# Optimization experiments

Measured on AMD Instinct MI355X. Metric: run time of the kernel, lower is better.

Reference implementation:

```python
import jax, jax.numpy as jnp
import numpy as np

U10_IDX, V10_IDX = 0, 1
WIND_THRESH = 0.5


def _gru(x, h, Wih, Whh, bih, bhh):
    # standard torch GRUCell math
    gi = x @ Wih.T + bih
    gh = h @ Whh.T + bhh
    ir, iz, inn = jnp.split(gi, 3, axis=-1)
    hr, hz, hnn = jnp.split(gh, 3, axis=-1)
    r = jax.nn.sigmoid(ir + hr)
    z = jax.nn.sigmoid(iz + hz)
    n = jnp.tanh(inn + r * hnn)
    return (1.0 - z) * n + z * h


def setup_inputs() -> dict:
    B, N, H, F, Th, Tf = 256, 184, 128, 8, 24, 24
    key = jax.random.key(0)
    ks = jax.random.split(key, 24)
    s = 0.1
    f32 = jnp.float32
    feature = jax.random.normal(ks[0], (B, Th + Tf, N, F), f32)
    pm25_hist = jax.random.uniform(ks[1], (B, Th, N, 1), dtype=f32)
    adj_mat = (jax.random.uniform(ks[2], (N, N)) < 0.1).astype(f32)
    angles = jax.random.uniform(ks[3], (N, N), f32, 0.0, 2.0 * np.pi)
    C = F + 1  # ChebConv in-channels = in_dim + out_dim
    return dict(
        feature=feature, pm25_hist=pm25_hist, adj_mat=adj_mat, angles=angles,
        W_ih_hist=s * jax.random.normal(ks[4], (3 * H, 2), f32),
        W_hh_hist=s * jax.random.normal(ks[5], (3 * H, H), f32),
        b_ih_hist=s * jax.random.normal(ks[6], (3 * H,), f32),
        b_hh_hist=s * jax.random.normal(ks[7], (3 * H,), f32),
        fc_hist_w=s * jax.random.normal(ks[8], (1, H), f32),
        fc_hist_b=s * jax.random.normal(ks[9], (1,), f32),
        cheb_w0=s * jax.random.normal(ks[10], (C, 1), f32),
        cheb_w1=s * jax.random.normal(ks[11], (C, 1), f32),
        cheb_b=s * jax.random.normal(ks[12], (1,), f32),
        W_ih=s * jax.random.normal(ks[13], (3 * H, C + 1), f32),
        W_hh=s * jax.random.normal(ks[14], (3 * H, H), f32),
        b_ih=s * jax.random.normal(ks[15], (3 * H,), f32),
        b_hh=s * jax.random.normal(ks[16], (3 * H,), f32),
        fc_out_w=s * jax.random.normal(ks[17], (1, H), f32),
        fc_out_b=s * jax.random.normal(ks[18], (1,), f32),
    )


def reference(feature, pm25_hist, adj_mat, angles,
              W_ih_hist, W_hh_hist, b_ih_hist, b_hh_hist,
              fc_hist_w, fc_hist_b,
              cheb_w0, cheb_w1, cheb_b,
              W_ih, W_hh, b_ih, b_hh,
              fc_out_w, fc_out_b):
    B, T, N, F = feature.shape
    H = W_hh.shape[1]
    Th = pm25_hist.shape[1]
    comp1 = jnp.cos(angles)                                # [N,N]
    comp2 = jnp.cos(angles - jnp.float32(np.pi / 2.0))     # [N,N]
    adj_b = adj_mat > 0

    # ---- history GRU over pm25_hist ----
    def hist_step(carry, p):
        hn, xn = carry
        x = jnp.concatenate([xn, p], axis=-1).reshape(B * N, 2)
        hn = _gru(x, hn, W_ih_hist, W_hh_hist, b_ih_hist, b_hh_hist)
        xn = hn.reshape(B, N, H) @ fc_hist_w.T + fc_hist_b
        return (hn, xn), None

    h0 = jnp.zeros((B * N, H), feature.dtype)
    x0 = jnp.zeros((B, N, 1), feature.dtype)
    (hn, xn), _ = jax.lax.scan(hist_step, (h0, x0), jnp.swapaxes(pm25_hist, 0, 1))

    # ---- forecast: dynamic wind-gated graph + ChebConv(K=2) + GRU ----
    def fore_step(carry, f):
        hn, xn = carry
        x = jnp.concatenate([xn, f], axis=-1)              # [B,N,F+1]
        u = f[..., U10_IDX]                                # [B,N]
        v = f[..., V10_IDX]
        wind = u[:, :, None] * comp1[None] + v[:, :, None] * comp2[None]
        # edge i->j iff adj and wind projection >= threshold
        M = jnp.logical_and(wind >= WIND_THRESH, adj_b[None]).astype(x.dtype)
        deg = M.sum(-1)                                    # source degree [B,N]
        has = deg > 0
        dinv = jnp.where(has, 1.0 / jnp.sqrt(jnp.where(has, deg, 1.0)), 0.0)
        # ChebConv scaled Laplacian (lambda_max=2, sym norm):
        # L_hat x [j] = -dinv_j * sum_i dinv_i * M[i,j] * x[i] + (0 if deg_j>0 else -1) * x[j]
        y = jnp.einsum('bij,bic->bjc', M * dinv[:, :, None], x)
        y = -dinv[:, :, None] * y + jnp.where(has, 0.0, -1.0)[:, :, None] * x
        g = jax.nn.sigmoid(x @ cheb_w0 + y @ cheb_w1 + cheb_b)  # [B,N,1]
        x2 = jnp.concatenate([x, g], axis=-1).reshape(B * N, F + 2)
        hn = _gru(x2, hn, W_ih, W_hh, b_ih, b_hh)
        xn = hn.reshape(B, N, H) @ fc_out_w.T + fc_out_b
        return (hn, xn), xn

    fore_feat = jnp.swapaxes(feature[:, Th:], 0, 1)        # [Tf,B,N,F]
    (_, _), preds = jax.lax.scan(fore_step, (hn, xn), fore_feat)
    return jnp.swapaxes(preds, 0, 1)                       # [B,Tf,N,1]
```

## Files before the change

### kernel.cpp

```cpp
#include <hip/hip_runtime.h>
#include <hip/hip_bf16.h>
#include <math.h>

#define BB 256
#define NN 184
#define HH 128
#define FF 8
#define TH 24
#define TF 24
#define KA 160
#define NG 512
#define RPAD 192
#define STRH 136
#define NT 1024
#define NW3 552
#define LOG2E 1.44269504088896f

#define REC_F 8832
#define REC_H 2944
#define OFF_DINV 4416
#define OFF_G 5152
#define OFF_AXF 5888

typedef __attribute__((ext_vector_type(8))) short bf16x8;
typedef __attribute__((ext_vector_type(4))) short bf16x4;
typedef __attribute__((ext_vector_type(4))) float f32x4;
typedef __attribute__((ext_vector_type(2))) unsigned u32x2;

#if __has_builtin(__builtin_amdgcn_mfma_f32_16x16x16bf16_1k)
#define XK16 1
#else
#define XK16 0
#endif

__host__ __device__ __forceinline__ long recOff(int b, int t) {
    const long PB = (long)TH * REC_H + (long)TF * REC_F;
    return (long)b * PB + ((t < TH) ? (long)t * REC_H
                                    : (long)TH * REC_H + (long)(t - TH) * REC_F);
}

__device__ __forceinline__ unsigned short f2bf(float f) {
    unsigned u = __float_as_uint(f);
    u += 0x7fffu + ((u >> 16) & 1u);
    return (unsigned short)(u >> 16);
}
__device__ __forceinline__ unsigned pkbf(float a, float b) {
    __hip_bfloat162 h = __float22bfloat162_rn(make_float2(a, b));
    return *reinterpret_cast<unsigned*>(&h);
}
__device__ __forceinline__ void gload16(const void* src, void* dst) {
    __builtin_amdgcn_global_load_lds(
        (const __attribute__((address_space(1))) unsigned int*)src,
        (__attribute__((address_space(3))) unsigned int*)dst, 16, 0, 0);
}

__global__ void prep_weights(const float* __restrict__ WhhH, const float* __restrict__ WihH,
                             const float* __restrict__ WhhF, const float* __restrict__ WihF,
                             const float* __restrict__ bihH, const float* __restrict__ bhhH,
                             const float* __restrict__ bihF, const float* __restrict__ bhhF,
                             unsigned short* __restrict__ WaH, unsigned short* __restrict__ WaF) {
    int idx = blockIdx.x * 256 + threadIdx.x;
    if (idx >= NG * KA) return;
    int jp = idx / KA, k = idx % KA;
    int j = jp & 127, part = jp >> 7;
    float vh = 0.f, vf = 0.f;
    if (part <= 1) {
        int row = part * 128 + j;
        if (k < 128) { vh = WhhH[row * 128 + k]; vf = WhhF[row * 128 + k]; }
        else {
            int s = k - 128;
            if (s == 0)  vh = WihH[row * 2 + 1];
            if (s < 8)   vf = WihF[row * 10 + (s + 1)];
            if (s == 8)  { vh = WihH[row * 2 + 0]; vf = WihF[row * 10 + 0]; }
            if (s == 9)  vf = WihF[row * 10 + 9];
            if (s == 11) { vh = bihH[row] + bhhH[row]; vf = bihF[row] + bhhF[row]; }
        }
    } else if (part == 2) {
        if (k < 128) { vh = WhhH[(256 + j) * 128 + k]; vf = WhhF[(256 + j) * 128 + k]; }
        else if (k == 139) { vh = bhhH[256 + j]; vf = bhhF[256 + j]; }
    } else {
        if (k >= 128) {
            int s = k - 128;
            if (s == 0)  vh = WihH[(256 + j) * 2 + 1];
            if (s < 8)   vf = WihF[(256 + j) * 10 + (s + 1)];
            if (s == 8)  { vh = WihH[(256 + j) * 2 + 0]; vf = WihF[(256 + j) * 10 + 0]; }
            if (s == 9)  vf = WihF[(256 + j) * 10 + 9];
            if (s == 11) { vh = bihH[256 + j]; vf = bihF[256 + j]; }
        }
    }
    float sc = (part <= 1) ? LOG2E : 2.0f * LOG2E;
    WaH[idx] = f2bf(vh * sc);
    WaF[idx] = f2bf(vf * sc);
}

__global__ void prep_edges(const float* __restrict__ angles, const float* __restrict__ adj,
                           float4* __restrict__ edges, int* __restrict__ cnt) {
    int idx = blockIdx.x * 256 + threadIdx.x;
    if (idx < NN * NN && adj[idx] > 0.f) {
        float a = angles[idx];
        int pos = atomicAdd(cnt, 1);
        float4 r;
        r.x = cosf(a);
        r.y = cosf(a - 1.57079632679489662f);
        r.z = __int_as_float(idx / NN);
        r.w = __int_as_float(idx % NN);
        edges[pos] = r;
    }
}

__global__ __launch_bounds__(256) void prep_graph(
    const float* __restrict__ feature, const float* __restrict__ pm25,
    const float4* __restrict__ edges, const int* __restrict__ ecnt,
    const float* __restrict__ cw0, const float* __restrict__ cw1,
    const float* __restrict__ cbb, char* __restrict__ xrec)
{
    const int bt = blockIdx.x;
    const int b = bt / (TH + TF), tt = bt % (TH + TF);
    const int tid = threadIdx.x;

    char* rec = xrec + recOff(b, tt);
    if (tt < TH) {
        if (tid < NN) {
            unsigned short pb = f2bf(pm25[((long)b * TH + tt) * NN + tid]);
            uint4* dst = (uint4*)rec + tid;
            *dst = make_uint4((unsigned)pb, 0u, 0u, 0u);
        }
        return;
    }

    __shared__ float f8[NN * FF];
    __shared__ unsigned long long mT[NN][3];
    __shared__ int dg[NN];
    __shared__ float di[NN];
    __shared__ float red[NW3][8];

    const float4* fb4 = (const float4*)(feature + ((long)b * (TH + TF) + tt) * (NN * FF));
    for (int i = tid; i < (NN * FF) / 4; i += 256) ((float4*)f8)[i] = fb4[i];
    for (int i = tid; i < NN * 3; i += 256) ((unsigned long long*)mT)[i] = 0ull;
    for (int i = tid; i < NN; i += 256) dg[i] = 0;
    __syncthreads();
    const int nE = *ecnt;
    for (int e = tid; e < nE; e += 256) {
        float4 r = edges[e];
        int ii = __float_as_int(r.z), jj = __float_as_int(r.w);
        if (f8[ii * FF] * r.x + f8[ii * FF + 1] * r.y >= 0.5f) {
            atomicAdd(&dg[ii], 1);
            atomicOr(&mT[jj][ii >> 6], 1ull << (ii & 63));
        }
    }
    __syncthreads();
    if (tid < NN) di[tid] = (dg[tid] > 0) ? rsqrtf((float)dg[tid]) : 0.f;
    __syncthreads();
    unsigned long long* mr = (unsigned long long*)rec;
    for (int i = tid; i < NW3; i += 256) mr[i] = ((const unsigned long long*)mT)[i];
    for (int task = tid; task < NW3; task += 256) {
        int j = task / 3, wd = task - j * 3;
        unsigned long long m = mT[j][wd];
        float acc[8];
        #pragma unroll
        for (int c = 0; c < 8; ++c) acc[c] = 0.f;
        while (m) {
            int bp = __ffsll(m) - 1; m &= m - 1;
            int i = wd * 64 + bp;
            float d = di[i];
            #pragma unroll
            for (int c = 0; c < 8; ++c) acc[c] += d * f8[i * FF + c];
        }
        #pragma unroll
        for (int c = 0; c < 8; ++c) red[task][c] = acc[c];
    }
    __syncthreads();
    if (tid < NN) {
        int j = tid;
        float dj = di[j];
        float hzj = (dj > 0.f) ? 0.f : -1.f;
        float G = cbb[0];
        #pragma unroll
        for (int c = 0; c < 8; ++c) {
            float accc = red[j * 3 + 0][c] + red[j * 3 + 1][c] + red[j * 3 + 2][c];
            float xv = f8[j * FF + c];
            float y = -dj * accc + hzj * xv;
            G += xv * cw0[c + 1] + y * cw1[c + 1];
        }
        ((float*)(rec + OFF_DINV))[j] = dj;
        ((float*)(rec + OFF_G))[j] = G;
        unsigned short* ax = (unsigned short*)(rec + OFF_AXF) + j * 8;
        #pragma unroll
        for (int c = 0; c < 8; ++c) ax[c] = f2bf(f8[j * FF + c]);
    }
}

__global__ __launch_bounds__(NT, 4) void fused_dgc(
    const unsigned short* __restrict__ WaH,
    const unsigned short* __restrict__ WaF,
    const float* __restrict__ fchw, const float* __restrict__ fchb,
    const float* __restrict__ fcow, const float* __restrict__ fcob,
    const float* __restrict__ cw0, const float* __restrict__ cw1,
    const char* __restrict__ xrec,
    float* __restrict__ pred)
{
    __shared__ unsigned short Ah[2][RPAD * STRH];
    __shared__ unsigned short AxR[RPAD * 8];
    __shared__ __align__(16) char stg[2][8960];
    __shared__ float red_s[RPAD * 9];
    __shared__ float2 dx_s[NN];
    __shared__ float fcls_f[132];
    __shared__ unsigned short zero16[8];

    const int tid = threadIdx.x;
    const int bb = blockIdx.x;
    const int w = tid >> 6, lane = tid & 63, q = lane >> 4, lq = lane & 15;
    const int cg = w & 7, rh = w >> 3;

    for (int i = tid; i < RPAD * STRH; i += NT) Ah[0][i] = 0;
    for (int i = tid; i < RPAD * 8; i += NT)
        AxR[i] = ((i & 7) == 3) ? (unsigned short)0x3F80 : (unsigned short)0;
    if (tid < 8) zero16[tid] = 0;
    if (tid < NN) dx_s[tid] = make_float2(0.f, 0.f);

    bf16x8 wregH[3][4];
#if XK16
    bf16x4 wregX[4];
#else
    bf16x8 wregX[4];
#endif
    auto load_phase = [&](const unsigned short* Wa, const float* fcw, const float* fcb) {
        const int jcol = cg * 16 + lq;
        #pragma unroll
        for (int g = 0; g < 3; ++g)
            #pragma unroll
            for (int kc = 0; kc < 4; ++kc)
                wregH[g][kc] = *(const bf16x8*)(Wa + (long)(g * 128 + jcol) * KA + kc * 32 + q * 8);
        #pragma unroll
        for (int g = 0; g < 4; ++g)
#if XK16
            wregX[g] = *(const bf16x4*)(Wa + (long)(g * 128 + jcol) * KA + 128 + q * 4);
#else
            wregX[g] = *(const bf16x8*)(Wa + (long)(g * 128 + jcol) * KA + 128 + q * 8);
#endif
        if (tid < 132) fcls_f[tid] = (tid < 128) ? fcw[tid] : ((tid == 128) ? fcb[0] : 0.f);
    };
    load_phase(WaH, fchw, fchb);

    if (tid < NN)
        gload16(xrec + recOff(bb, 0) + (long)tid * 16,
                (char*)stg[0] + OFF_AXF + (tid & ~63) * 16);

    const float w00 = cw0[0], w10 = cw1[0];

    int p = 0;
    __syncthreads();

    for (int t = 0; t < TH + TF; ++t) {
        const unsigned long long* maskS = (const unsigned long long*)stg[p];
        const float* GS = (const float*)(stg[p] + OFF_G);
        const unsigned short* AxFS = (const unsigned short*)(stg[p] + OFF_AXF);

        if (t >= TH) {
            const int jg = tid >> 2, wd = tid & 3;
            if (jg < NN) {
                unsigned long long m = (wd < 3) ? maskS[jg * 3 + wd] : 0ull;
                float acc = 0.f;
                while (m) {
                    int bp = __ffsll(m) - 1; m &= m - 1;
                    float2 dxv = dx_s[wd * 64 + bp];
                    acc += dxv.x * dxv.y;
                }
                acc += __shfl_xor(acc, 1);
                acc += __shfl_xor(acc, 2);
                if (wd == 0) {
                    float2 dxj = dx_s[jg];
                    float hzj = (dxj.x > 0.f) ? 0.f : -1.f;
                    float y0 = -dxj.x * acc + hzj * dxj.y;
                    float pre = GS[jg] + dxj.y * w00 + y0 * w10;
                    float g = __builtin_amdgcn_rcpf(1.0f + exp2f(-LOG2E * pre));
                    AxR[jg * 8 + 1] = f2bf(g);
                }
            }
            __syncthreads();
        }

        const int t2 = t + 1;
        if (t2 < TH + TF) {
            const int nch = (t2 < TH) ? NN : NW3;
            if (tid < nch)
                gload16(xrec + recOff(bb, t2) + (long)tid * 16,
                        (char*)stg[p ^ 1] + ((t2 < TH) ? OFF_AXF : 0) + (tid & ~63) * 16);
        }

        f32x4 fw = *(const f32x4*)&fcls_f[cg * 16 + q * 4];
        #pragma unroll
        for (int rl = 0; rl < 6; ++rl) {
            const int row = rh * 96 + rl * 16 + lq;
            const int ro = row * STRH;
            f32x4 a0 = {0.f,0.f,0.f,0.f}, a1 = {0.f,0.f,0.f,0.f}, a2 = {0.f,0.f,0.f,0.f};
            #pragma unroll
            for (int kc = 0; kc < 4; ++kc) {
                bf16x8 bh = *(const bf16x8*)(&Ah[p][ro + kc * 32 + q * 8]);
                a0 = __builtin_amdgcn_mfma_f32_16x16x32_bf16(wregH[0][kc], bh, a0, 0, 0, 0);
                a1 = __builtin_amdgcn_mfma_f32_16x16x32_bf16(wregH[1][kc], bh, a1, 0, 0, 0);
                a2 = __builtin_amdgcn_mfma_f32_16x16x32_bf16(wregH[2][kc], bh, a2, 0, 0, 0);
            }
            f32x4 a3 = {0.f,0.f,0.f,0.f};
#if XK16
            const unsigned short* bxp = (q < 2) ? (AxFS + row * 8 + q * 4)
                                      : (q == 2) ? (AxR + row * 8) : zero16;
            bf16x4 bx = *(const bf16x4*)bxp;
            a0 = __builtin_amdgcn_mfma_f32_16x16x16bf16_1k(wregX[0], bx, a0, 0, 0, 0);
            a1 = __builtin_amdgcn_mfma_f32_16x16x16bf16_1k(wregX[1], bx, a1, 0, 0, 0);
            a2 = __builtin_amdgcn_mfma_f32_16x16x16bf16_1k(wregX[2], bx, a2, 0, 0, 0);
            a3 = __builtin_amdgcn_mfma_f32_16x16x16bf16_1k(wregX[3], bx, a3, 0, 0, 0);
#else
            const unsigned short* bxp = (q == 0) ? (AxFS + row * 8)
                                      : (q == 1) ? (AxR + row * 8) : zero16;
            bf16x8 bx = *(const bf16x8*)bxp;
            a0 = __builtin_amdgcn_mfma_f32_16x16x32_bf16(wregX[0], bx, a0, 0, 0, 0);
            a1 = __builtin_amdgcn_mfma_f32_16x16x32_bf16(wregX[1], bx, a1, 0, 0, 0);
            a2 = __builtin_amdgcn_mfma_f32_16x16x32_bf16(wregX[2], bx, a2, 0, 0, 0);
            a3 = __builtin_amdgcn_mfma_f32_16x16x32_bf16(wregX[3], bx, a3, 0, 0, 0);
#endif

            u32x2 hold = *(const u32x2*)&Ah[p][ro + cg * 16 + q * 4];

            float hn[4];
            #pragma unroll
            for (int rg = 0; rg < 4; ++rg) {
                unsigned hu = hold[rg >> 1];
                float ho = ((rg & 1) == 0) ? __uint_as_float(hu << 16)
                                           : __uint_as_float(hu & 0xffff0000u);
                float rr = __builtin_amdgcn_rcpf(1.0f + exp2f(-a0[rg]));
                float zz = __builtin_amdgcn_rcpf(1.0f + exp2f(-a1[rg]));
                float wv = fmaf(rr, a2[rg], a3[rg]);
                unsigned sg = __float_as_uint(wv) & 0x80000000u;
                float e = exp2f(-fabsf(wv));
                float tv = (1.0f - e) * __builtin_amdgcn_rcpf(1.0f + e);
                tv = __uint_as_float(__float_as_uint(tv) ^ sg);
                hn[rg] = fmaf(zz, ho - tv, tv);
            }
            float pf = hn[0] * fw.x + hn[1] * fw.y + hn[2] * fw.z + hn[3] * fw.w;
            pf += __shfl_xor(pf, 16);
            pf += __shfl_xor(pf, 32);
            u32x2 pk;
            pk[0] = pkbf(hn[0], hn[1]);
            pk[1] = pkbf(hn[2], hn[3]);
            *(u32x2*)&Ah[p ^ 1][ro + cg * 16 + q * 4] = pk;
            if (q == 0) red_s[row * 9 + cg] = pf;
        }
        __syncthreads();

        if (tid < NN) {
            float xn = fcls_f[128];
            #pragma unroll
            for (int c = 0; c < 8; ++c) xn += red_s[tid * 9 + c];
            float dv = 0.f;
            if (t2 >= TH && t2 < TH + TF)
                dv = *(const float*)(stg[p ^ 1] + OFF_DINV + tid * 4);
            dx_s[tid] = make_float2(dv, xn);
            AxR[tid * 8 + 0] = f2bf(xn);
            if (t >= TH) pred[((long)bb * TF + (t - TH)) * NN + tid] = xn;
        }
        __syncthreads();

        if (t == TH - 1)
            load_phase(WaF, fcow, fcob);
        p ^= 1;
    }
}

extern "C" void kernel_launch(void* const* d_in, const int* in_sizes, int n_in,
                              void* d_out, int out_size, void* d_ws, size_t ws_size,
                              hipStream_t stream) {
    const float* feature = (const float*)d_in[0];
    const float* pm25    = (const float*)d_in[1];
    const float* adj     = (const float*)d_in[2];
    const float* angles  = (const float*)d_in[3];
    const float* W_ih_h  = (const float*)d_in[4];
    const float* W_hh_h  = (const float*)d_in[5];
    const float* b_ih_h  = (const float*)d_in[6];
    const float* b_hh_h  = (const float*)d_in[7];
    const float* fch_w   = (const float*)d_in[8];
    const float* fch_b   = (const float*)d_in[9];
    const float* cw0     = (const float*)d_in[10];
    const float* cw1     = (const float*)d_in[11];
    const float* cbb     = (const float*)d_in[12];
    const float* W_ih    = (const float*)d_in[13];
    const float* W_hh    = (const float*)d_in[14];
    const float* b_ih    = (const float*)d_in[15];
    const float* b_hh    = (const float*)d_in[16];
    const float* fco_w   = (const float*)d_in[17];
    const float* fco_b   = (const float*)d_in[18];
    float* pred = (float*)d_out;

    char* ws = (char*)d_ws;
    size_t off = 0;
    unsigned short* WaH   = (unsigned short*)(ws + off); off += (size_t)NG * KA * 2;
    unsigned short* WaF   = (unsigned short*)(ws + off); off += (size_t)NG * KA * 2;
    float4*         edges = (float4*)(ws + off);         off += (size_t)NN * NN * 16;
    int*            cnt   = (int*)(ws + off);            off += 16;
    char*           xrec  = (char*)(ws + off);
    off += (size_t)BB * ((size_t)TH * REC_H + (size_t)TF * REC_F);

    hipMemsetAsync(cnt, 0, 16, stream);
    prep_weights<<<(NG * KA + 255) / 256, 256, 0, stream>>>(
        W_hh_h, W_ih_h, W_hh, W_ih, b_ih_h, b_hh_h, b_ih, b_hh, WaH, WaF);
    prep_edges<<<(NN * NN + 255) / 256, 256, 0, stream>>>(angles, adj, edges, cnt);
    prep_graph<<<BB * (TH + TF), 256, 0, stream>>>(
        feature, pm25, edges, cnt, cw0, cw1, cbb, xrec);

    fused_dgc<<<BB, NT, 0, stream>>>(
        WaH, WaF, fch_w, fch_b, fco_w, fco_b, cw0, cw1, xrec, pred);
}
```

Measured before the change: 691.7 us.

## Fold history fc projection into GRU weights and skip per-step reduction

During the history phase, the fc_hist output feeding back into the next GRU input is folded algebraically into the recurrent weights (Whh + Wih[:,0]·fc_w, with a bias correction and a first-step correction term). This removes the per-step fc dot product, shuffle reduction and extra barrier for history steps. The n-gate's input part needs a separate fourth weight group with extra MFMAs. Pm25 history is staged once into LDS in compact bf16 instead of being streamed per step, and exp2 uses the hardware builtin. The folded weights are rounded to bf16, which may change numerical error.

```diff
diff --git a/kernel.cpp b/kernel.cpp
--- a/kernel.cpp
+++ b/kernel.cpp
@@ -9,7 +9,7 @@
 #define TH 24
 #define TF 24
 #define KA 160
-#define NG 512
+#define NG2 640
 #define RPAD 192
 #define STRH 136
 #define NT 1024
@@ -17,7 +17,6 @@
 #define LOG2E 1.44269504088896f
 
 #define REC_F 8832
-#define REC_H 2944
 #define OFF_DINV 4416
 #define OFF_G 5152
 #define OFF_AXF 5888
@@ -33,11 +32,11 @@
 #define XK16 0
 #endif
 
-__host__ __device__ __forceinline__ long recOff(int b, int t) {
-    const long PB = (long)TH * REC_H + (long)TF * REC_F;
-    return (long)b * PB + ((t < TH) ? (long)t * REC_H
-                                    : (long)TH * REC_H + (long)(t - TH) * REC_F);
-}
+#if __has_builtin(__builtin_amdgcn_exp2f)
+#define EXP2(x) __builtin_amdgcn_exp2f(x)
+#else
+#define EXP2(x) exp2f(x)
+#endif
 
 __device__ __forceinline__ unsigned short f2bf(float f) {
     unsigned u = __float_as_uint(f);
@@ -58,35 +57,46 @@
                              const float* __restrict__ WhhF, const float* __restrict__ WihF,
                              const float* __restrict__ bihH, const float* __restrict__ bhhH,
                              const float* __restrict__ bihF, const float* __restrict__ bhhF,
+                             const float* __restrict__ fchw, const float* __restrict__ fchb,
                              unsigned short* __restrict__ WaH, unsigned short* __restrict__ WaF) {
     int idx = blockIdx.x * 256 + threadIdx.x;
-    if (idx >= NG * KA) return;
+    if (idx >= NG2 * KA) return;
     int jp = idx / KA, k = idx % KA;
     int j = jp & 127, part = jp >> 7;
     float vh = 0.f, vf = 0.f;
     if (part <= 1) {
         int row = part * 128 + j;
-        if (k < 128) { vh = WhhH[row * 128 + k]; vf = WhhF[row * 128 + k]; }
-        else {
+        if (k < 128) {
+            vh = WhhH[row * 128 + k] + WihH[row * 2 + 0] * fchw[k];
+            vf = WhhF[row * 128 + k];
+        } else {
             int s = k - 128;
             if (s == 0)  vh = WihH[row * 2 + 1];
             if (s < 8)   vf = WihF[row * 10 + (s + 1)];
             if (s == 8)  { vh = WihH[row * 2 + 0]; vf = WihF[row * 10 + 0]; }
             if (s == 9)  vf = WihF[row * 10 + 9];
-            if (s == 11) { vh = bihH[row] + bhhH[row]; vf = bihF[row] + bhhF[row]; }
+            if (s == 11) {
+                vh = bihH[row] + bhhH[row] + WihH[row * 2 + 0] * fchb[0];
+                vf = bihF[row] + bhhF[row];
+            }
         }
     } else if (part == 2) {
         if (k < 128) { vh = WhhH[(256 + j) * 128 + k]; vf = WhhF[(256 + j) * 128 + k]; }
         else if (k == 139) { vh = bhhH[256 + j]; vf = bhhF[256 + j]; }
-    } else {
+    } else if (part == 3) {
         if (k >= 128) {
             int s = k - 128;
             if (s == 0)  vh = WihH[(256 + j) * 2 + 1];
             if (s < 8)   vf = WihF[(256 + j) * 10 + (s + 1)];
             if (s == 8)  { vh = WihH[(256 + j) * 2 + 0]; vf = WihF[(256 + j) * 10 + 0]; }
             if (s == 9)  vf = WihF[(256 + j) * 10 + 9];
-            if (s == 11) { vh = bihH[256 + j]; vf = bihF[256 + j]; }
-        }
+            if (s == 11) {
+                vh = bihH[256 + j] + WihH[(256 + j) * 2 + 0] * fchb[0];
+                vf = bihF[256 + j];
+            }
+        }
+    } else {
+        if (k < 128) vh = WihH[(256 + j) * 2 + 0] * fchw[k];
     }
     float sc = (part <= 1) ? LOG2E : 2.0f * LOG2E;
     WaH[idx] = f2bf(vh * sc);
@@ -112,21 +122,21 @@
     const float* __restrict__ feature, const float* __restrict__ pm25,
     const float4* __restrict__ edges, const int* __restrict__ ecnt,
     const float* __restrict__ cw0, const float* __restrict__ cw1,
-    const float* __restrict__ cbb, char* __restrict__ xrec)
+    const float* __restrict__ cbb, char* __restrict__ xrec,
+    unsigned short* __restrict__ phist)
 {
     const int bt = blockIdx.x;
     const int b = bt / (TH + TF), tt = bt % (TH + TF);
     const int tid = threadIdx.x;
 
-    char* rec = xrec + recOff(b, tt);
     if (tt < TH) {
-        if (tid < NN) {
-            unsigned short pb = f2bf(pm25[((long)b * TH + tt) * NN + tid]);
-            uint4* dst = (uint4*)rec + tid;
-            *dst = make_uint4((unsigned)pb, 0u, 0u, 0u);
-        }
+        if (tid < NN)
+            phist[(long)b * (TH * NN) + tt * NN + tid] =
+                f2bf(pm25[((long)b * TH + tt) * NN + tid]);
         return;
     }
+
+    char* rec = xrec + ((long)b * TF + (tt - TH)) * REC_F;
 
     __shared__ float f8[NN * FF];
     __shared__ unsigned long long mT[NN][3];
@@ -196,7 +206,7 @@
     const float* __restrict__ fchw, const float* __restrict__ fchb,
     const float* __restrict__ fcow, const float* __restrict__ fcob,
     const float* __restrict__ cw0, const float* __restrict__ cw1,
-    const char* __restrict__ xrec,
+    const char* __restrict__ xrec, const unsigned short* __restrict__ phist,
     float* __restrict__ pred)
 {
     __shared__ unsigned short Ah[2][RPAD * STRH];
@@ -206,6 +216,7 @@
     __shared__ float2 dx_s[NN];
     __shared__ float fcls_f[132];
     __shared__ unsigned short zero16[8];
+    __shared__ __align__(16) unsigned short phist_s[TH * NN + 16];
 
     const int tid = threadIdx.x;
     const int bb = blockIdx.x;
@@ -218,19 +229,23 @@
     if (tid < 8) zero16[tid] = 0;
     if (tid < NN) dx_s[tid] = make_float2(0.f, 0.f);
 
-    bf16x8 wregH[3][4];
+    bf16x8 wregH[4][4];
 #if XK16
     bf16x4 wregX[4];
 #else
     bf16x8 wregX[4];
 #endif
-    auto load_phase = [&](const unsigned short* Wa, const float* fcw, const float* fcb) {
+    auto load_w = [&](const unsigned short* Wa, const float* fcw, const float* fcb, bool h4) {
         const int jcol = cg * 16 + lq;
         #pragma unroll
         for (int g = 0; g < 3; ++g)
             #pragma unroll
             for (int kc = 0; kc < 4; ++kc)
                 wregH[g][kc] = *(const bf16x8*)(Wa + (long)(g * 128 + jcol) * KA + kc * 32 + q * 8);
+        if (h4)
+            #pragma unroll
+            for (int kc = 0; kc < 4; ++kc)
+                wregH[3][kc] = *(const bf16x8*)(Wa + (long)(4 * 128 + jcol) * KA + kc * 32 + q * 8);
         #pragma unroll
         for (int g = 0; g < 4; ++g)
 #if XK16
@@ -240,23 +255,26 @@
 #endif
         if (tid < 132) fcls_f[tid] = (tid < 128) ? fcw[tid] : ((tid == 128) ? fcb[0] : 0.f);
     };
-    load_phase(WaH, fchw, fchb);
-
-    if (tid < NN)
-        gload16(xrec + recOff(bb, 0) + (long)tid * 16,
-                (char*)stg[0] + OFF_AXF + (tid & ~63) * 16);
+    load_w(WaH, fchw, fchb, true);
+
+    if (tid < NW3)
+        gload16((const char*)phist + (long)bb * (TH * NN * 2) + tid * 16,
+                (char*)phist_s + (tid & ~63) * 16);
 
     const float w00 = cw0[0], w10 = cw1[0];
+    const float fcbH = fchb[0];
 
     int p = 0;
     __syncthreads();
 
     for (int t = 0; t < TH + TF; ++t) {
-        const unsigned long long* maskS = (const unsigned long long*)stg[p];
-        const float* GS = (const float*)(stg[p] + OFF_G);
+        const bool hist = (t < TH);
+        const bool dofc = (t >= TH - 1);
         const unsigned short* AxFS = (const unsigned short*)(stg[p] + OFF_AXF);
 
-        if (t >= TH) {
+        if (!hist) {
+            const unsigned long long* maskS = (const unsigned long long*)stg[p];
+            const float* GS = (const float*)(stg[p] + OFF_G);
             const int jg = tid >> 2, wd = tid & 3;
             if (jg < NN) {
                 unsigned long long m = (wd < 3) ? maskS[jg * 3 + wd] : 0ull;
@@ -273,7 +291,7 @@
                     float hzj = (dxj.x > 0.f) ? 0.f : -1.f;
                     float y0 = -dxj.x * acc + hzj * dxj.y;
                     float pre = GS[jg] + dxj.y * w00 + y0 * w10;
-                    float g = __builtin_amdgcn_rcpf(1.0f + exp2f(-LOG2E * pre));
+                    float g = __builtin_amdgcn_rcpf(1.0f + EXP2(-LOG2E * pre));
                     AxR[jg * 8 + 1] = f2bf(g);
                 }
             }
@@ -281,39 +299,57 @@
         }
 
         const int t2 = t + 1;
-        if (t2 < TH + TF) {
-            const int nch = (t2 < TH) ? NN : NW3;
-            if (tid < nch)
-                gload16(xrec + recOff(bb, t2) + (long)tid * 16,
-                        (char*)stg[p ^ 1] + ((t2 < TH) ? OFF_AXF : 0) + (tid & ~63) * 16);
-        }
+        if (t2 >= TH && t2 < TH + TF && tid < NW3)
+            gload16(xrec + ((long)bb * TF + (t2 - TH)) * REC_F + tid * 16,
+                    (char*)stg[p ^ 1] + (tid & ~63) * 16);
 
         f32x4 fw = *(const f32x4*)&fcls_f[cg * 16 + q * 4];
+        const unsigned short corr0 = (t == 0) ? f2bf(-fcbH) : (unsigned short)0;
         #pragma unroll
         for (int rl = 0; rl < 6; ++rl) {
             const int row = rh * 96 + rl * 16 + lq;
             const int ro = row * STRH;
             f32x4 a0 = {0.f,0.f,0.f,0.f}, a1 = {0.f,0.f,0.f,0.f}, a2 = {0.f,0.f,0.f,0.f};
+            f32x4 a3 = {0.f,0.f,0.f,0.f};
             #pragma unroll
             for (int kc = 0; kc < 4; ++kc) {
                 bf16x8 bh = *(const bf16x8*)(&Ah[p][ro + kc * 32 + q * 8]);
                 a0 = __builtin_amdgcn_mfma_f32_16x16x32_bf16(wregH[0][kc], bh, a0, 0, 0, 0);
                 a1 = __builtin_amdgcn_mfma_f32_16x16x32_bf16(wregH[1][kc], bh, a1, 0, 0, 0);
                 a2 = __builtin_amdgcn_mfma_f32_16x16x32_bf16(wregH[2][kc], bh, a2, 0, 0, 0);
-            }
-            f32x4 a3 = {0.f,0.f,0.f,0.f};
+                if (hist)
+                    a3 = __builtin_amdgcn_mfma_f32_16x16x32_bf16(wregH[3][kc], bh, a3, 0, 0, 0);
+            }
 #if XK16
-            const unsigned short* bxp = (q < 2) ? (AxFS + row * 8 + q * 4)
-                                      : (q == 2) ? (AxR + row * 8) : zero16;
-            bf16x4 bx = *(const bf16x4*)bxp;
+            bf16x4 bx;
+            if (hist) {
+                unsigned short pb = phist_s[t * NN + row];
+                bf16x4 z = {0,0,0,0};
+                bx = z;
+                if (q == 0) bx[0] = (short)pb;
+                if (q == 2) { bx[0] = (short)corr0; bx[3] = (short)0x3F80; }
+            } else {
+                const unsigned short* bxp = (q < 2) ? (AxFS + row * 8 + q * 4)
+                                          : (q == 2) ? (AxR + row * 8) : zero16;
+                bx = *(const bf16x4*)bxp;
+            }
             a0 = __builtin_amdgcn_mfma_f32_16x16x16bf16_1k(wregX[0], bx, a0, 0, 0, 0);
             a1 = __builtin_amdgcn_mfma_f32_16x16x16bf16_1k(wregX[1], bx, a1, 0, 0, 0);
             a2 = __builtin_amdgcn_mfma_f32_16x16x16bf16_1k(wregX[2], bx, a2, 0, 0, 0);
             a3 = __builtin_amdgcn_mfma_f32_16x16x16bf16_1k(wregX[3], bx, a3, 0, 0, 0);
 #else
-            const unsigned short* bxp = (q == 0) ? (AxFS + row * 8)
-                                      : (q == 1) ? (AxR + row * 8) : zero16;
-            bf16x8 bx = *(const bf16x8*)bxp;
+            bf16x8 bx;
+            if (hist) {
+                unsigned short pb = phist_s[t * NN + row];
+                bf16x8 z = {0,0,0,0,0,0,0,0};
+                bx = z;
+                if (q == 0) bx[0] = (short)pb;
+                if (q == 1) { bx[0] = (short)corr0; bx[3] = (short)0x3F80; }
+            } else {
+                const unsigned short* bxp = (q == 0) ? (AxFS + row * 8)
+                                          : (q == 1) ? (AxR + row * 8) : zero16;
+                bx = *(const bf16x8*)bxp;
+            }
             a0 = __builtin_amdgcn_mfma_f32_16x16x32_bf16(wregX[0], bx, a0, 0, 0, 0);
             a1 = __builtin_amdgcn_mfma_f32_16x16x32_bf16(wregX[1], bx, a1, 0, 0, 0);
             a2 = __builtin_amdgcn_mfma_f32_16x16x32_bf16(wregX[2], bx, a2, 0, 0, 0);
@@ -328,41 +364,45 @@
                 unsigned hu = hold[rg >> 1];
                 float ho = ((rg & 1) == 0) ? __uint_as_float(hu << 16)
                                            : __uint_as_float(hu & 0xffff0000u);
-                float rr = __builtin_amdgcn_rcpf(1.0f + exp2f(-a0[rg]));
-                float zz = __builtin_amdgcn_rcpf(1.0f + exp2f(-a1[rg]));
+                float rr = __builtin_amdgcn_rcpf(1.0f + EXP2(-a0[rg]));
+                float zz = __builtin_amdgcn_rcpf(1.0f + EXP2(-a1[rg]));
                 float wv = fmaf(rr, a2[rg], a3[rg]);
                 unsigned sg = __float_as_uint(wv) & 0x80000000u;
-                float e = exp2f(-fabsf(wv));
+                float e = EXP2(-fabsf(wv));
                 float tv = (1.0f - e) * __builtin_amdgcn_rcpf(1.0f + e);
                 tv = __uint_as_float(__float_as_uint(tv) ^ sg);
                 hn[rg] = fmaf(zz, ho - tv, tv);
             }
-            float pf = hn[0] * fw.x + hn[1] * fw.y + hn[2] * fw.z + hn[3] * fw.w;
-            pf += __shfl_xor(pf, 16);
-            pf += __shfl_xor(pf, 32);
             u32x2 pk;
             pk[0] = pkbf(hn[0], hn[1]);
             pk[1] = pkbf(hn[2], hn[3]);
             *(u32x2*)&Ah[p ^ 1][ro + cg * 16 + q * 4] = pk;
-            if (q == 0) red_s[row * 9 + cg] = pf;
+            if (dofc) {
+                float pf = hn[0] * fw.x + hn[1] * fw.y + hn[2] * fw.z + hn[3] * fw.w;
+                pf += __shfl_xor(pf, 16);
+                pf += __shfl_xor(pf, 32);
+                if (q == 0) red_s[row * 9 + cg] = pf;
+            }
         }
         __syncthreads();
 
-        if (tid < NN) {
-            float xn = fcls_f[128];
-            #pragma unroll
-            for (int c = 0; c < 8; ++c) xn += red_s[tid * 9 + c];
-            float dv = 0.f;
-            if (t2 >= TH && t2 < TH + TF)
-                dv = *(const float*)(stg[p ^ 1] + OFF_DINV + tid * 4);
-            dx_s[tid] = make_float2(dv, xn);
-            AxR[tid * 8 + 0] = f2bf(xn);
-            if (t >= TH) pred[((long)bb * TF + (t - TH)) * NN + tid] = xn;
-        }
-        __syncthreads();
+        if (dofc) {
+            if (tid < NN) {
+                float xn = fcls_f[128];
+                #pragma unroll
+                for (int c = 0; c < 8; ++c) xn += red_s[tid * 9 + c];
+                float dv = 0.f;
+                if (t2 >= TH && t2 < TH + TF)
+                    dv = *(const float*)(stg[p ^ 1] + OFF_DINV + tid * 4);
+                dx_s[tid] = make_float2(dv, xn);
+                AxR[tid * 8 + 0] = f2bf(xn);
+                if (t >= TH) pred[((long)bb * TF + (t - TH)) * NN + tid] = xn;
+            }
+            __syncthreads();
+        }
 
         if (t == TH - 1)
-            load_phase(WaF, fcow, fcob);
+            load_w(WaF, fcow, fcob, false);
         p ^= 1;
     }
 }
@@ -393,20 +433,22 @@
 
     char* ws = (char*)d_ws;
     size_t off = 0;
-    unsigned short* WaH   = (unsigned short*)(ws + off); off += (size_t)NG * KA * 2;
-    unsigned short* WaF   = (unsigned short*)(ws + off); off += (size_t)NG * KA * 2;
+    unsigned short* WaH   = (unsigned short*)(ws + off); off += (size_t)NG2 * KA * 2;
+    unsigned short* WaF   = (unsigned short*)(ws + off); off += (size_t)NG2 * KA * 2;
     float4*         edges = (float4*)(ws + off);         off += (size_t)NN * NN * 16;
     int*            cnt   = (int*)(ws + off);            off += 16;
+    unsigned short* phist = (unsigned short*)(ws + off); off += (size_t)BB * TH * NN * 2;
     char*           xrec  = (char*)(ws + off);
-    off += (size_t)BB * ((size_t)TH * REC_H + (size_t)TF * REC_F);
+    off += (size_t)BB * TF * REC_F;
 
     hipMemsetAsync(cnt, 0, 16, stream);
-    prep_weights<<<(NG * KA + 255) / 256, 256, 0, stream>>>(
-        W_hh_h, W_ih_h, W_hh, W_ih, b_ih_h, b_hh_h, b_ih, b_hh, WaH, WaF);
+    prep_weights<<<(NG2 * KA + 255) / 256, 256, 0, stream>>>(
+        W_hh_h, W_ih_h, W_hh, W_ih, b_ih_h, b_hh_h, b_ih, b_hh, fch_w, fch_b,
+        WaH, WaF);
     prep_edges<<<(NN * NN + 255) / 256, 256, 0, stream>>>(angles, adj, edges, cnt);
     prep_graph<<<BB * (TH + TF), 256, 0, stream>>>(
-        feature, pm25, edges, cnt, cw0, cw1, cbb, xrec);
+        feature, pm25, edges, cnt, cw0, cw1, cbb, xrec, phist);
 
     fused_dgc<<<BB, NT, 0, stream>>>(
-        WaH, WaF, fch_w, fch_b, fco_w, fco_b, cw0, cw1, xrec, pred);
-}
+        WaH, WaF, fch_w, fch_b, fco_w, fco_b, cw0, cw1, xrec, phist, pred);
+}
```

Result: faster. 645.0 us (-6.7%).
